# Kernel tuning notes

Measured on AMD Instinct MI355X. Metric: run time of the kernel, lower is better.

Reference implementation:

```python
import jax, jax.numpy as jnp
import numpy as np

N = 4096
D = 1024          # latent_vector_size
H, KD, VD = 16, 64, 64
MHK = H * KD      # 1024
MHV = H * VD      # 1024
HID = D // 2      # 512
EPS = 1e-5


def _layernorm(v, g, b):
    mu = jnp.mean(v, axis=-1, keepdims=True)
    var = jnp.mean(jnp.square(v - mu), axis=-1, keepdims=True)
    return (v - mu) * jax.lax.rsqrt(var + EPS) * g + b


def setup_inputs() -> dict:
    key = jax.random.key(0)
    ks = jax.random.split(key, 12)
    s = lambda fan_in: 1.0 / np.sqrt(fan_in)
    return {
        "x": jax.random.normal(ks[0], (N, D), dtype=jnp.float32),
        "w_qkv": jax.random.uniform(ks[1], (D, H * (2 * KD + VD)), jnp.float32, -s(D), s(D)),
        "b_qkv": jax.random.uniform(ks[2], (H * (2 * KD + VD),), jnp.float32, -s(D), s(D)),
        "w_msa": jax.random.uniform(ks[3], (MHV, D), jnp.float32, -s(MHV), s(MHV)),
        "b_msa": jax.random.uniform(ks[4], (D,), jnp.float32, -s(MHV), s(MHV)),
        "ln_g": jnp.ones((D,), jnp.float32),
        "ln_b": jnp.zeros((D,), jnp.float32),
        "w_h1": jax.random.uniform(ks[5], (D, HID), jnp.float32, -s(D), s(D)),
        "b_h1": jax.random.uniform(ks[6], (HID,), jnp.float32, -s(D), s(D)),
        "w_h2": jax.random.uniform(ks[7], (HID, D), jnp.float32, -s(HID), s(HID)),
        "b_h2": jax.random.uniform(ks[8], (D,), jnp.float32, -s(HID), s(HID)),
    }


def reference(x, w_qkv, b_qkv, w_msa, b_msa, ln_g, ln_b, w_h1, b_h1, w_h2, b_h2):
    # --- attention block (note: heads are never split; one big [N,N] softmax) ---
    ln1 = _layernorm(x, ln_g, ln_b)                       # [N, D]
    qkv = ln1 @ w_qkv + b_qkv                             # [N, 3*MHK]
    q, k, v = qkv[:, :MHK], qkv[:, MHK:2 * MHK], qkv[:, 2 * MHK:]
    scores = (q @ k.T) / jnp.sqrt(jnp.float32(KD))        # [N, N]
    attn = jax.nn.softmax(scores, axis=-1)
    mha = (attn @ v) @ w_msa + b_msa                      # [N, D]
    enc1 = x + mha
    # --- MLP block (shared layernorm params; softmax output, residual) ---
    ln2 = _layernorm(enc1, ln_g, ln_b)
    h1 = jax.nn.gelu(ln2 @ w_h1 + b_h1, approximate=False)  # [N, HID]
    h2 = jax.nn.gelu(h1 @ w_h2 + b_h2, approximate=False)   # [N, D]
    out = jax.nn.softmax(h2, axis=-1)                        # nn.Softmax() -> dim=1 for 2D
    return enc1 + out
```

## Files before the change

kernel.cpp:

```cpp
#include <hip/hip_runtime.h>
#include <stdint.h>

#define DEV __device__ __forceinline__

typedef unsigned short u16;
typedef __attribute__((ext_vector_type(8))) unsigned short u16x8;
typedef __attribute__((ext_vector_type(4))) unsigned short u16x4;
typedef __attribute__((ext_vector_type(4))) float f32x4;

DEV float bf2f(u16 u) { return __uint_as_float(((unsigned)u) << 16); }
DEV u16 f2bf(float f) {
  unsigned u = __float_as_uint(f);
  u += 0x7FFFu + ((u >> 16) & 1u);
  return (u16)(u >> 16);
}
DEV float gelu_exact(float v) { return 0.5f * v * (1.0f + erff(v * 0.70710678118654752f)); }

__global__ __launch_bounds__(256) void transpose_f32_bf16(
    const float* __restrict__ in, u16* __restrict__ out, int rows, int cols) {
  __shared__ float t[32][33];
  const int tx = threadIdx.x, ty = threadIdx.y;
  const int c0 = blockIdx.x * 32, r0 = blockIdx.y * 32;
#pragma unroll
  for (int i = 0; i < 32; i += 8) t[ty + i][tx] = in[(size_t)(r0 + ty + i) * cols + c0 + tx];
  __syncthreads();
#pragma unroll
  for (int i = 0; i < 32; i += 8)
    out[(size_t)(c0 + ty + i) * rows + r0 + tx] = f2bf(t[tx][ty + i]);
}

__global__ __launch_bounds__(256) void transpose_bf16(
    const u16* __restrict__ in, int ldin, u16* __restrict__ out, int ldout) {
  __shared__ u16 t[32][33];
  const int tx = threadIdx.x, ty = threadIdx.y;
  const int c0 = blockIdx.x * 32, r0 = blockIdx.y * 32;
#pragma unroll
  for (int i = 0; i < 32; i += 8) t[ty + i][tx] = in[(size_t)(r0 + ty + i) * ldin + c0 + tx];
  __syncthreads();
#pragma unroll
  for (int i = 0; i < 32; i += 8)
    out[(size_t)(c0 + ty + i) * ldout + r0 + tx] = t[tx][ty + i];
}

__global__ __launch_bounds__(256) void layernorm_bf16(
    const float* __restrict__ in, const float* __restrict__ g,
    const float* __restrict__ b, u16* __restrict__ out) {
  const int tid = threadIdx.x;
  const int lane = tid & 63, wid = tid >> 6;
  const size_t base = (size_t)blockIdx.x * 1024;
  const float4 v = ((const float4*)(in + base))[tid];
  float s = v.x + v.y + v.z + v.w;
  float ss = v.x * v.x + v.y * v.y + v.z * v.z + v.w * v.w;
#pragma unroll
  for (int off = 32; off > 0; off >>= 1) {
    s += __shfl_down(s, off);
    ss += __shfl_down(ss, off);
  }
  __shared__ float red[8];
  if (lane == 0) { red[wid] = s; red[4 + wid] = ss; }
  __syncthreads();
  s = red[0] + red[1] + red[2] + red[3];
  ss = red[4] + red[5] + red[6] + red[7];
  const float mu = s * (1.0f / 1024.0f);
  const float inv = rsqrtf(ss * (1.0f / 1024.0f) - mu * mu + 1e-5f);
  const float4 gv = ((const float4*)g)[tid];
  const float4 bv = ((const float4*)b)[tid];
  u16x4 o;
  o.x = f2bf((v.x - mu) * inv * gv.x + bv.x);
  o.y = f2bf((v.y - mu) * inv * gv.y + bv.y);
  o.z = f2bf((v.z - mu) * inv * gv.z + bv.z);
  o.w = f2bf((v.w - mu) * inv * gv.w + bv.w);
  *(u16x4*)(out + base + tid * 4) = o;
}

__global__ __launch_bounds__(256) void softmax4096(u16* __restrict__ p) {
  const int tid = threadIdx.x;
  const int lane = tid & 63, wid = tid >> 6;
  u16* row = p + (size_t)blockIdx.x * 4096;
  u16x8 r0 = ((u16x8*)row)[tid * 2];
  u16x8 r1 = ((u16x8*)row)[tid * 2 + 1];
  float v[16];
#pragma unroll
  for (int i = 0; i < 8; ++i) { v[i] = bf2f(r0[i]); v[8 + i] = bf2f(r1[i]); }
  float mx = v[0];
#pragma unroll
  for (int i = 1; i < 16; ++i) mx = fmaxf(mx, v[i]);
#pragma unroll
  for (int off = 32; off > 0; off >>= 1) mx = fmaxf(mx, __shfl_down(mx, off));
  __shared__ float red[8];
  if (lane == 0) red[wid] = mx;
  __syncthreads();
  mx = fmaxf(fmaxf(red[0], red[1]), fmaxf(red[2], red[3]));
  float sum = 0.0f;
#pragma unroll
  for (int i = 0; i < 16; ++i) { v[i] = __expf(v[i] - mx); sum += v[i]; }
#pragma unroll
  for (int off = 32; off > 0; off >>= 1) sum += __shfl_down(sum, off);
  if (lane == 0) red[4 + wid] = sum;
  __syncthreads();
  sum = red[4] + red[5] + red[6] + red[7];
  const float inv = 1.0f / sum;
  u16x8 o0, o1;
#pragma unroll
  for (int i = 0; i < 8; ++i) { o0[i] = f2bf(v[i] * inv); o1[i] = f2bf(v[8 + i] * inv); }
  ((u16x8*)row)[tid * 2] = o0;
  ((u16x8*)row)[tid * 2 + 1] = o1;
}

__global__ __launch_bounds__(256) void final_softmax_add(
    const float* __restrict__ h2, const float* __restrict__ enc1, float* __restrict__ out) {
  const int tid = threadIdx.x;
  const int lane = tid & 63, wid = tid >> 6;
  const size_t base = (size_t)blockIdx.x * 1024;
  float4 v = ((const float4*)(h2 + base))[tid];
  float mx = fmaxf(fmaxf(v.x, v.y), fmaxf(v.z, v.w));
#pragma unroll
  for (int off = 32; off > 0; off >>= 1) mx = fmaxf(mx, __shfl_down(mx, off));
  __shared__ float red[8];
  if (lane == 0) red[wid] = mx;
  __syncthreads();
  mx = fmaxf(fmaxf(red[0], red[1]), fmaxf(red[2], red[3]));
  v.x = __expf(v.x - mx); v.y = __expf(v.y - mx);
  v.z = __expf(v.z - mx); v.w = __expf(v.w - mx);
  float sum = v.x + v.y + v.z + v.w;
#pragma unroll
  for (int off = 32; off > 0; off >>= 1) sum += __shfl_down(sum, off);
  if (lane == 0) red[4 + wid] = sum;
  __syncthreads();
  sum = red[4] + red[5] + red[6] + red[7];
  const float inv = 1.0f / sum;
  const float4 e = ((const float4*)(enc1 + base))[tid];
  float4 o;
  o.x = e.x + v.x * inv; o.y = e.y + v.y * inv;
  o.z = e.z + v.z * inv; o.w = e.w + v.w * inv;
  ((float4*)(out + base))[tid] = o;
}

template <int EPI>
__global__ __launch_bounds__(256) void gemm_bt(
    const u16* __restrict__ A, int lda, const u16* __restrict__ Bt, int ldb,
    void* __restrict__ Cv, int ldc, const float* __restrict__ bias,
    const float* __restrict__ xres, int ldx, float scale, int K) {
  __shared__ alignas(16) u16 As[128 * 32];
  __shared__ alignas(16) u16 Bs[128 * 32];
  const int tid = threadIdx.x;
  const int wid = tid >> 6;
  const int lane = tid & 63;
  const int m0 = blockIdx.y * 128;
  const int n0 = blockIdx.x * 128;
  const int wr = wid >> 1, wc = wid & 1;

  const int srow = lane >> 2;
  const int sseg = (lane & 3) * 8;

  f32x4 acc[4][4];
#pragma unroll
  for (int m = 0; m < 4; ++m)
#pragma unroll
    for (int n = 0; n < 4; ++n) { f32x4 z = {0.f, 0.f, 0.f, 0.f}; acc[m][n] = z; }

  const int arow = wr * 64 + (lane & 15);
  const int brow = wc * 64 + (lane & 15);
  const int koff = (lane >> 4) * 8;

  for (int k0 = 0; k0 < K; k0 += 32) {
#pragma unroll
    for (int i = 0; i < 2; ++i) {
      const int r = i * 64 + wid * 16;
      const u16* ga = A + (size_t)(m0 + r + srow) * lda + k0 + sseg;
      const u16* gb = Bt + (size_t)(n0 + r + srow) * ldb + k0 + sseg;
      __builtin_amdgcn_global_load_lds((__attribute__((address_space(1))) void*)ga,
                                       (__attribute__((address_space(3))) void*)&As[r * 32], 16, 0, 0);
      __builtin_amdgcn_global_load_lds((__attribute__((address_space(1))) void*)gb,
                                       (__attribute__((address_space(3))) void*)&Bs[r * 32], 16, 0, 0);
    }
    __syncthreads();
    u16x8 a[4], b[4];
#pragma unroll
    for (int m = 0; m < 4; ++m) a[m] = *(const u16x8*)&As[(arow + m * 16) * 32 + koff];
#pragma unroll
    for (int n = 0; n < 4; ++n) b[n] = *(const u16x8*)&Bs[(brow + n * 16) * 32 + koff];
#pragma unroll
    for (int m = 0; m < 4; ++m)
#pragma unroll
      for (int n = 0; n < 4; ++n)
        asm("v_mfma_f32_16x16x32_bf16 %0, %1, %2, %0" : "+v"(acc[m][n]) : "v"(a[m]), "v"(b[n]));
    __syncthreads();
  }

  const int crow0 = m0 + wr * 64 + ((lane >> 4) << 2);
  const int ccol0 = n0 + wc * 64 + (lane & 15);
#pragma unroll
  for (int m = 0; m < 4; ++m) {
#pragma unroll
    for (int n = 0; n < 4; ++n) {
      const int col = ccol0 + n * 16;
      float bia = 0.0f;
      if (EPI == 1 || EPI == 3 || EPI == 4 || EPI == 5) bia = bias[col];
#pragma unroll
      for (int r = 0; r < 4; ++r) {
        const int row = crow0 + m * 16 + r;
        const float v = acc[m][n][r];
        if (EPI == 0) {
          ((u16*)Cv)[(size_t)row * ldc + col] = f2bf(v * scale);
        } else if (EPI == 1) {
          ((u16*)Cv)[(size_t)row * ldc + col] = f2bf(v + bia);
        } else if (EPI == 2) {
          ((u16*)Cv)[(size_t)row * ldc + col] = f2bf(v);
        } else if (EPI == 3) {
          ((float*)Cv)[(size_t)row * ldc + col] = v + bia + xres[(size_t)row * ldx + col];
        } else if (EPI == 4) {
          ((u16*)Cv)[(size_t)row * ldc + col] = f2bf(gelu_exact(v + bia));
        } else {
          ((float*)Cv)[(size_t)row * ldc + col] = gelu_exact(v + bia);
        }
      }
    }
  }
}

extern "C" void kernel_launch(void* const* d_in, const int* in_sizes, int n_in,
                              void* d_out, int out_size, void* d_ws, size_t ws_size,
                              hipStream_t stream) {
  const float* x     = (const float*)d_in[0];
  const float* w_qkv = (const float*)d_in[1];
  const float* b_qkv = (const float*)d_in[2];
  const float* w_msa = (const float*)d_in[3];
  const float* b_msa = (const float*)d_in[4];
  const float* ln_g  = (const float*)d_in[5];
  const float* ln_b  = (const float*)d_in[6];
  const float* w_h1  = (const float*)d_in[7];
  const float* b_h1  = (const float*)d_in[8];
  const float* w_h2  = (const float*)d_in[9];
  const float* b_h2  = (const float*)d_in[10];

  char* w = (char*)d_ws;
  u16*   qkv   = (u16*)(w + 0);
  u16*   sc    = (u16*)(w + 25165824);
  u16*   lnb   = (u16*)(w + 58720256);
  u16*   av    = (u16*)(w + 67108864);
  u16*   vT    = (u16*)(w + 75497472);
  float* enc1  = (float*)(w + 83886080);
  u16*   h1    = (u16*)(w + 100663296);
  float* h2    = (float*)(w + 104857600);
  u16*   wqkvT = (u16*)(w + 121634816);
  u16*   wmsaT = (u16*)(w + 127926272);
  u16*   wh1T  = (u16*)(w + 130023424);
  u16*   wh2T  = (u16*)(w + 131072000);
  (void)in_sizes; (void)n_in; (void)out_size; (void)ws_size;

  dim3 tb(32, 8);
  transpose_f32_bf16<<<dim3(96, 32), tb, 0, stream>>>(w_qkv, wqkvT, 1024, 3072);
  transpose_f32_bf16<<<dim3(32, 32), tb, 0, stream>>>(w_msa, wmsaT, 1024, 1024);
  transpose_f32_bf16<<<dim3(16, 32), tb, 0, stream>>>(w_h1, wh1T, 1024, 512);
  transpose_f32_bf16<<<dim3(32, 16), tb, 0, stream>>>(w_h2, wh2T, 512, 1024);

  layernorm_bf16<<<4096, 256, 0, stream>>>(x, ln_g, ln_b, lnb);
  gemm_bt<1><<<dim3(24, 32), 256, 0, stream>>>(lnb, 1024, wqkvT, 1024, qkv, 3072,
                                               b_qkv, nullptr, 0, 1.0f, 1024);
  transpose_bf16<<<dim3(32, 128), tb, 0, stream>>>(qkv + 2048, 3072, vT, 4096);
  gemm_bt<0><<<dim3(32, 32), 256, 0, stream>>>(qkv, 3072, qkv + 1024, 3072, sc, 4096,
                                               nullptr, nullptr, 0, 0.125f, 1024);
  softmax4096<<<4096, 256, 0, stream>>>(sc);
  gemm_bt<2><<<dim3(8, 32), 256, 0, stream>>>(sc, 4096, vT, 4096, av, 1024,
                                              nullptr, nullptr, 0, 1.0f, 4096);
  gemm_bt<3><<<dim3(8, 32), 256, 0, stream>>>(av, 1024, wmsaT, 1024, enc1, 1024,
                                              b_msa, x, 1024, 1.0f, 1024);
  layernorm_bf16<<<4096, 256, 0, stream>>>(enc1, ln_g, ln_b, lnb);
  gemm_bt<4><<<dim3(4, 32), 256, 0, stream>>>(lnb, 1024, wh1T, 1024, h1, 512,
                                              b_h1, nullptr, 0, 1.0f, 1024);
  gemm_bt<5><<<dim3(8, 32), 256, 0, stream>>>(h1, 512, wh2T, 512, h2, 1024,
                                              b_h2, nullptr, 0, 1.0f, 512);
  final_softmax_add<<<4096, 256, 0, stream>>>(h2, enc1, (float*)d_out);
}
```

Before: 285.4 us.

## Triple-buffer GEMM LDS loads, swizzle LDS layout, and remap workgroups

Turns the bf16 MFMA GEMM main loop into a three-stage pipeline. Global-to-LDS loads for tile k+2 are issued while tile k is computed, and each iteration ends with a counted vmcnt wait plus a barrier instead of two __syncthreads. It also XOR-swizzles the LDS column segments to cut bank conflicts on the fragment reads, and remaps workgroup IDs across eight groups to improve L2 locality. The costs are triple the LDS footprint, which may lower occupancy, and some redundant loads of the last tile at the tail. Correctness relies on the gridDim product being divisible by 8 and on the hand-written waitcnt count.

```diff
diff --git a/kernel.cpp b/kernel.cpp
--- a/kernel.cpp
+++ b/kernel.cpp
@@ -141,17 +141,22 @@
     const u16* __restrict__ A, int lda, const u16* __restrict__ Bt, int ldb,
     void* __restrict__ Cv, int ldc, const float* __restrict__ bias,
     const float* __restrict__ xres, int ldx, float scale, int K) {
-  __shared__ alignas(16) u16 As[128 * 32];
-  __shared__ alignas(16) u16 Bs[128 * 32];
+  __shared__ alignas(16) u16 As[3][128 * 32];
+  __shared__ alignas(16) u16 Bs[3][128 * 32];
   const int tid = threadIdx.x;
   const int wid = tid >> 6;
   const int lane = tid & 63;
-  const int m0 = blockIdx.y * 128;
-  const int n0 = blockIdx.x * 128;
+
+  const int gx = gridDim.x;
+  const int nwg = gridDim.x * gridDim.y;
+  int wg = blockIdx.y * gx + blockIdx.x;
+  wg = (wg & 7) * (nwg >> 3) + (wg >> 3);
+  const int m0 = (wg / gx) * 128;
+  const int n0 = (wg % gx) * 128;
   const int wr = wid >> 1, wc = wid & 1;
 
   const int srow = lane >> 2;
-  const int sseg = (lane & 3) * 8;
+  const int sseg = (((lane & 3) ^ ((lane >> 3) & 3))) * 8;
 
   f32x4 acc[4][4];
 #pragma unroll
@@ -161,31 +166,48 @@
 
   const int arow = wr * 64 + (lane & 15);
   const int brow = wc * 64 + (lane & 15);
-  const int koff = (lane >> 4) * 8;
-
-  for (int k0 = 0; k0 < K; k0 += 32) {
+  const int koff = (((lane >> 4) ^ ((lane >> 1) & 3))) * 8;
+
+  const int NT = K >> 5;
+
+  auto STAGE = [&](int kt, int buf) {
+    const int k0 = kt * 32;
 #pragma unroll
     for (int i = 0; i < 2; ++i) {
       const int r = i * 64 + wid * 16;
       const u16* ga = A + (size_t)(m0 + r + srow) * lda + k0 + sseg;
       const u16* gb = Bt + (size_t)(n0 + r + srow) * ldb + k0 + sseg;
       __builtin_amdgcn_global_load_lds((__attribute__((address_space(1))) void*)ga,
-                                       (__attribute__((address_space(3))) void*)&As[r * 32], 16, 0, 0);
+                                       (__attribute__((address_space(3))) void*)&As[buf][r * 32], 16, 0, 0);
       __builtin_amdgcn_global_load_lds((__attribute__((address_space(1))) void*)gb,
-                                       (__attribute__((address_space(3))) void*)&Bs[r * 32], 16, 0, 0);
+                                       (__attribute__((address_space(3))) void*)&Bs[buf][r * 32], 16, 0, 0);
     }
-    __syncthreads();
+  };
+
+  STAGE(0, 0);
+  STAGE(1, 1);
+  asm volatile("s_waitcnt vmcnt(4)" ::: "memory");
+  __builtin_amdgcn_s_barrier();
+
+  int cur = 0;
+  for (int t = 0; t < NT; ++t) {
+    const int kt = (t + 2 < NT) ? (t + 2) : (NT - 1);
+    STAGE(kt, (cur + 2) % 3);
+
     u16x8 a[4], b[4];
 #pragma unroll
-    for (int m = 0; m < 4; ++m) a[m] = *(const u16x8*)&As[(arow + m * 16) * 32 + koff];
-#pragma unroll
-    for (int n = 0; n < 4; ++n) b[n] = *(const u16x8*)&Bs[(brow + n * 16) * 32 + koff];
+    for (int m = 0; m < 4; ++m) a[m] = *(const u16x8*)&As[cur][(arow + m * 16) * 32 + koff];
+#pragma unroll
+    for (int n = 0; n < 4; ++n) b[n] = *(const u16x8*)&Bs[cur][(brow + n * 16) * 32 + koff];
 #pragma unroll
     for (int m = 0; m < 4; ++m)
 #pragma unroll
       for (int n = 0; n < 4; ++n)
         asm("v_mfma_f32_16x16x32_bf16 %0, %1, %2, %0" : "+v"(acc[m][n]) : "v"(a[m]), "v"(b[n]));
-    __syncthreads();
+
+    asm volatile("s_waitcnt vmcnt(4)" ::: "memory");
+    __builtin_amdgcn_s_barrier();
+    cur = (cur + 1) % 3;
   }
 
   const int crow0 = m0 + wr * 64 + ((lane >> 4) << 2);
```

Result: no change. 282.5 us (-1.0%).
